# Performance work log

Measured on AMD Instinct MI355X. Metric: run time of the kernel, lower is better.

The kernel has to match this reference:

```python
import jax, jax.numpy as jnp
import numpy as np

N_SAMPLES = 256   # n_samples from __init__
N_THIN = 10       # N from __init__
N_WORDS = 4096


def setup_inputs() -> dict:
    key = jax.random.key(0)
    k1, k2, k3 = jax.random.split(key, 3)
    # scale potentials so per-step weight deltas stay in a sane exp() range
    bigram = jax.random.normal(k1, (N_WORDS, N_WORDS), dtype=jnp.float32)
    start = jax.random.normal(k2, (N_WORDS,), dtype=jnp.float32)
    end = jax.random.normal(k3, (N_WORDS,), dtype=jnp.float32)
    return {"n_words": N_WORDS, "bigram": bigram, "start": start, "end": end}


def _mh_chain(bigram, start, end, n_words, chain_size, rng):
    # chain[0] = identity permutation (random_start=False)
    perm0 = jnp.arange(n_words, dtype=jnp.int32)
    w0 = bigram[perm0[:-1], perm0[1:]].sum() + start[perm0[0]] + end[perm0[-1]]

    def step(carry, k):
        perm, w_last = carry
        k_pos, k_cat, k_u = jax.random.split(k, 3)
        # pick a token to move, remove it -> perm2 of length n_words-1
        pos = jax.random.randint(k_pos, (), 0, n_words)
        to_move = perm[pos]
        j = jnp.arange(n_words - 1)
        perm2 = perm[j + (j >= pos).astype(j.dtype)]
        # insertion logits over n_words slots (self._probs, unnormalized log p)
        logits = jnp.zeros((n_words,), dtype=bigram.dtype)
        logits = logits.at[0].add(start[to_move]).at[-1].add(end[to_move])
        logits = logits.at[1:].add(bigram[perm2, to_move])   # left-neighbor term
        logits = logits.at[:-1].add(bigram[to_move, perm2])  # right-neighbor term
        p = jax.nn.softmax(logits)
        new_pos = jax.random.categorical(k_cat, logits)
        # insert to_move at new_pos
        jj = jnp.arange(n_words)
        shifted = perm2[jnp.clip(jj - (jj > new_pos).astype(jj.dtype), 0, n_words - 2)]
        sample = jnp.where(jj == new_pos, to_move, shifted).astype(perm.dtype)
        # new chain weight
        new_w = bigram[sample[:-1], sample[1:]].sum() + start[sample[0]] + end[sample[-1]]
        # MH accept ratio; removing to_move from sample recovers perm2, so the
        # reverse insertion distribution equals p -> ratio p[new_pos]/p[pos]
        acc = jnp.minimum(1.0, jnp.exp(new_w - w_last) * p[new_pos] / p[pos])
        accept = acc > jax.random.uniform(k_u, ())
        perm_next = jnp.where(accept, sample, perm)
        w_next = jnp.where(accept, new_w, w_last)
        return (perm_next, w_next), perm_next

    keys = jax.random.split(rng, chain_size - 1)
    _, perms = jax.lax.scan(step, (perm0, w0), keys)
    chain = jnp.concatenate([perm0[None, :], perms], axis=0)  # [chain_size, n_words]
    sel = jnp.arange(0, chain_size, N_THIN) + (N_THIN - 1)    # thin: every N-th state
    return chain[sel]


def reference(n_words, bigram, start, end):
    chain_size = N_SAMPLES * N_THIN
    rng = jax.random.key(42)
    return _mh_chain(bigram, start, end, n_words, chain_size, rng)
```

## Files before the change

kernel.cpp:

```cpp
#include <hip/hip_runtime.h>
#include <stdint.h>


#define NW 4096
#define NSTEPS 2559
#define NTHREADS 1024
#define NWAVES 16

typedef unsigned long long u64;
typedef uint32_t u32;
typedef unsigned short u16;

__device__ __forceinline__ u32 rotl32(u32 v, u32 r) { return (v << r) | (v >> (32u - r)); }

__device__ __forceinline__ void tf2x32(u32 k0, u32 k1, u32 x0, u32 x1, u32* o0, u32* o1) {
  u32 ks2 = k0 ^ k1 ^ 0x1BD11BDAu;
  x0 += k0; x1 += k1;
#define TFR(r0, r1, r2, r3)                      \
  x0 += x1; x1 = rotl32(x1, r0); x1 ^= x0;       \
  x0 += x1; x1 = rotl32(x1, r1); x1 ^= x0;       \
  x0 += x1; x1 = rotl32(x1, r2); x1 ^= x0;       \
  x0 += x1; x1 = rotl32(x1, r3); x1 ^= x0;
  TFR(13, 15, 26, 6)  x0 += k1;  x1 += ks2 + 1u;
  TFR(17, 29, 16, 24) x0 += ks2; x1 += k0 + 2u;
  TFR(13, 15, 26, 6)  x0 += k0;  x1 += k1 + 3u;
  TFR(17, 29, 16, 24) x0 += k1;  x1 += ks2 + 4u;
  TFR(13, 15, 26, 6)  x0 += ks2; x1 += k0 + 5u;
#undef TFR
  *o0 = x0; *o1 = x1;
}

__device__ __forceinline__ float unif01(u32 bits) {
  return __uint_as_float((bits >> 9) | 0x3f800000u) - 1.0f;
}

__device__ __forceinline__ u32 fkey(float f) {
  u32 b = __float_as_uint(f);
  return b ^ ((b >> 31) ? 0xFFFFFFFFu : 0x80000000u);
}


template <int CTRL>
__device__ __forceinline__ u32 dpp32(u32 v) {
  return (u32)__builtin_amdgcn_update_dpp(0, (int)v, CTRL, 0xF, 0xF, true);
}

template <int CTRL>
__device__ __forceinline__ void dppmax64(u32& hi, u32& lo) {
  u32 h2 = dpp32<CTRL>(hi);
  u32 l2 = dpp32<CTRL>(lo);
  bool g = (h2 > hi) || (h2 == hi && l2 > lo);
  hi = g ? h2 : hi;
  lo = g ? l2 : lo;
}

__device__ __forceinline__ u64 wave_max_u64(u64 key) {
  u32 lo = (u32)key, hi = (u32)(key >> 32);
  dppmax64<0x111>(hi, lo); dppmax64<0x112>(hi, lo);
  dppmax64<0x114>(hi, lo); dppmax64<0x118>(hi, lo);
  dppmax64<0x142>(hi, lo); dppmax64<0x143>(hi, lo);
  return ((u64)hi << 32) | lo;
}

__device__ __forceinline__ u64 bfly16_max_u64(u64 key) {
  u32 lo = (u32)key, hi = (u32)(key >> 32);
  dppmax64<0xB1>(hi, lo); dppmax64<0x4E>(hi, lo);
  dppmax64<0x141>(hi, lo); dppmax64<0x140>(hi, lo);
  return ((u64)hi << 32) | lo;
}


#define TT 32
__global__ void transpose_k(const float* __restrict__ in, float* __restrict__ out) {
  __shared__ float tile[TT][TT + 1];
  int x = blockIdx.x * TT + threadIdx.x;
  int y = blockIdx.y * TT + threadIdx.y;
  for (int j = 0; j < TT; j += 8) tile[threadIdx.y + j][threadIdx.x] = in[(u64)(y + j) * NW + x];
  __syncthreads();
  x = blockIdx.y * TT + threadIdx.x;
  y = blockIdx.x * TT + threadIdx.y;
  for (int j = 0; j < TT; j += 8) out[(u64)(y + j) * NW + x] = tile[threadIdx.x][threadIdx.y + j];
}

__global__ void gumbel_k(float* __restrict__ gumb) {
  long long idx = (long long)blockIdx.x * blockDim.x + threadIdx.x;
  if (idx >= (long long)NSTEPS * NW) return;
  int t = (int)(idx >> 12);
  int i = (int)(idx & (NW - 1));
  u32 kt0, kt1, kc0, kc1, ba, bb;
  tf2x32(0u, 42u, 0u, (u32)t, &kt0, &kt1);
  tf2x32(kt0, kt1, 0u, 1u, &kc0, &kc1);
  tf2x32(kc0, kc1, 0u, (u32)i, &ba, &bb);
  float u = unif01(ba ^ bb);
  if (u == 0.0f) u = 1.17549435e-38f;
  float t1 = (float)log((double)u);
  float t2 = (float)log((double)(-t1));
  gumb[idx] = -t2;
}

__global__ void posu_k(int* __restrict__ posArr, float* __restrict__ uArr) {
  int t = blockIdx.x * blockDim.x + threadIdx.x;
  if (t >= NSTEPS) return;
  u32 kt0, kt1, kp0, kp1, ku0, ku1, k2a, k2b, ra, rb, ua, ub;
  tf2x32(0u, 42u, 0u, (u32)t, &kt0, &kt1);
  tf2x32(kt0, kt1, 0u, 0u, &kp0, &kp1);
  tf2x32(kt0, kt1, 0u, 2u, &ku0, &ku1);
  tf2x32(kp0, kp1, 0u, 1u, &k2a, &k2b);
  tf2x32(k2a, k2b, 0u, 0u, &ra, &rb);
  posArr[t] = (int)((ra ^ rb) & (u32)(NW - 1));
  tf2x32(ku0, ku1, 0u, 0u, &ua, &ub);
  uArr[t] = unif01(ua ^ ub);
}


#define SAMPLE_AT(idx)                                                        \
  ((idx) < np ? (int)s_perm[(idx) + ((idx) >= pos)]                           \
              : ((idx) == np ? tm                                             \
                             : (int)s_perm[((idx)-1) + (((idx)-1) >= pos)]))

__global__ __launch_bounds__(NTHREADS)
void mcmc_fast13(const float* __restrict__ bigram,
                 const float* __restrict__ bigT,
                 const float* __restrict__ gumb,
                 const int* __restrict__ posArr,
                 const float* __restrict__ uArr,
                 const float* __restrict__ startv,
                 const float* __restrict__ endv,
                 int* __restrict__ out) {
  __shared__ u16    s_perm[NW];
  __shared__ float2 s_rows[NW];
  __shared__ float  s_pairw[NW];
  __shared__ u64    s_redu[NWAVES];
  __shared__ float  s_stm, s_etm, s_lpos, s_brgS, s_vn1, s_vn2;
  __shared__ int    s_accs, s_tmA;

  const int tid = threadIdx.x;
  const int lane = tid & 63;
  const int wid = tid >> 6;
  const int j0 = tid * 4;

  for (int i = tid; i < NW; i += NTHREADS) s_perm[i] = (u16)i;
  ushort4 pq = make_ushort4((u16)j0, (u16)(j0 + 1), (u16)(j0 + 2), (u16)(j0 + 3));
  float4 pwq;
  pwq.x = bigram[(u64)j0 * NW + (j0 + 1)];
  pwq.y = bigram[(u64)(j0 + 1) * NW + (j0 + 2)];
  pwq.z = bigram[(u64)(j0 + 2) * NW + (j0 + 3)];
  pwq.w = (j0 + 3 < NW - 1) ? bigram[(u64)(j0 + 3) * NW + (j0 + 4)] : 0.0f;
  ((float4*)s_pairw)[tid] = pwq;

  int pos = posArr[0];
  int pn1 = posArr[1];
  float u_cur = uArr[0];
  float un1 = uArr[1];
  int tm = pos;
  {
    float4 rb4 = ((const float4*)(bigram + (u64)tm * NW))[tid];
    float4 rt4 = ((const float4*)(bigT + (u64)tm * NW))[tid];
    ((float4*)(&s_rows[j0]))[0] = make_float4(rt4.x, rb4.x, rt4.y, rb4.y);
    ((float4*)(&s_rows[j0]))[1] = make_float4(rt4.z, rb4.z, rt4.w, rb4.w);
  }
  if (tid == 0) { s_stm = startv[tm]; s_etm = endv[tm]; }

  float start_cur = startv[0];
  float end_cur = endv[NW - 1];

  float4 g4 = ((const float4*)gumb)[tid];
  __syncthreads();

  for (int t = 0; t < NSTEPS; ++t) {
    const float gg[4] = {g4.x, g4.y, g4.z, g4.w};
    const int tmR = (int)s_perm[pn1];
    const float4 rbR = ((const float4*)(bigram + (u64)tmR * NW))[tid];
    const float4 rtR = ((const float4*)(bigT + (u64)tmR * NW))[tid];
    float stmR = 0.0f, etmR = 0.0f;
    if (tid == 0) { stmR = startv[tmR]; etmR = endv[tmR]; }
    int pn2; float un2;
    {
      int tn = (t + 1 < NSTEPS) ? (t + 1) : (NSTEPS - 1);
      int tn2 = (t + 2 < NSTEPS) ? (t + 2) : (NSTEPS - 1);
      g4 = ((const float4*)(gumb + ((u64)tn << 12)))[tid];
      pn2 = posArr[tn2];
      un2 = uArr[tn2];
    }
    float stm_r = 0.0f, etm_r = 0.0f, remL = 0.0f, remR = 0.0f, brgv = 0.0f;
    float sv0m = 0.0f, ev1m = 0.0f;
    if (wid == 0) {
      stm_r = s_stm; etm_r = s_etm;
      int pl = (pos > 0) ? (int)s_perm[pos - 1] : 0;
      int pr = (pos < NW - 1) ? (int)s_perm[pos + 1] : 0;
      if (pos > 0)      remL = s_rows[pl].x;
      if (pos < NW - 1) remR = s_rows[pr].y;
      if (pos > 0 && pos < NW - 1) brgv = bigram[(u64)pl * NW + pr];
      sv0m = startv[(int)s_perm[(0 >= pos) ? 1 : 0]];
      ev1m = endv[(int)s_perm[(NW - 2) + ((NW - 2) >= pos)]];
      if (lane == 0) s_brgS = brgv;
    }

    const int p0i = pq.x, p1i = pq.y, p2i = pq.z, p3i = pq.w;
    int pm1, pp4;
    {
      u32 lo = (u32)pq.x | ((u32)pq.y << 16);
      u32 hi = (u32)pq.z | ((u32)pq.w << 16);
      pm1 = (int)(dpp32<0x138>(hi) >> 16);
      pp4 = (int)(dpp32<0x130>(lo) & 0xFFFFu);
      if (lane == 0)  pm1 = (tid > 0) ? (int)s_perm[j0 - 1] : 0;
      if (lane == 63) pp4 = (tid < NTHREADS - 1) ? (int)s_perm[j0 + 4] : 0;
    }
    float pwm1_e = 0.0f, pwp4_e = 0.0f;
    if (lane == 0 && tid > 0) pwm1_e = s_pairw[j0 - 1];
    if (lane == 63 && tid < NTHREADS - 1) pwp4_e = s_pairw[j0 + 4];

    const int w0 = (j0     >= pos) ? p1i : p0i;
    const int w1 = (j0 + 1 >= pos) ? p2i : p1i;
    const int w2 = (j0 + 2 >= pos) ? p3i : p2i;
    const int w3 = (j0 + 3 >= pos) ? pp4 : p3i;
    const int wprev = ((j0 - 1) >= pos) ? p0i : pm1;
    const float2 f0 = s_rows[w0];
    const float2 f1 = s_rows[w1];
    const float2 f2 = s_rows[w2];
    const float2 f3 = s_rows[w3];
    float tprev = __uint_as_float(dpp32<0x138>(__float_as_uint(f3.x)));
    if (lane == 0 && tid > 0) tprev = s_rows[wprev].x;
    float li0 = tprev + f0.y;
    float li1 = f0.x + f1.y;
    float li2 = f1.x + f2.y;
    float li3 = f2.x + f3.y;
    if (tid == 0)            li0 = s_stm + f0.y;
    if (tid == NTHREADS - 1) li3 = s_etm + f2.x;
    if ((pos >> 2) == tid) {
      int k = pos & 3;
      s_lpos = (k == 0) ? li0 : ((k == 1) ? li1 : ((k == 2) ? li2 : li3));
    }
    u64 best;
    {
      u64 b0 = ((u64)fkey(gg[0] + li0) << 32) | (u32)(NW - 1 - j0);
      u64 b1 = ((u64)fkey(gg[1] + li1) << 32) | (u32)(NW - 2 - j0);
      u64 b2 = ((u64)fkey(gg[2] + li2) << 32) | (u32)(NW - 3 - j0);
      u64 b3 = ((u64)fkey(gg[3] + li3) << 32) | (u32)(NW - 4 - j0);
      best = b0 > b1 ? b0 : b1;
      u64 b23 = b2 > b3 ? b2 : b3;
      if (b23 > best) best = b23;
    }
    best = wave_max_u64(best);
    if (lane == 63) s_redu[wid] = best;
    __syncthreads();

    if (wid == 0) {
      u64 bb = bfly16_max_u64(s_redu[lane & 15]);
      const int np = NW - 1 - (int)(bb & 0xFFFFFFFFu);
      int ls_i = (np >= 1) ? ((np - 1) + ((np - 1) >= pos)) : 0;
      int rs_i = (np <= NW - 2) ? (np + (np >= pos)) : 0;
      const int l_s = (int)s_perm[ls_i];
      const int r_s = (int)s_perm[rs_i];
      const int tmA = SAMPLE_AT(pn1);
      float splitv = 0.0f;
      if (np > 0 && np < NW - 1) {
        int k_s = (np - 1) + ((np - 1) >= pos);
        splitv = (np == pos) ? brgv : s_pairw[k_s];
      }
      float vnpm1 = (np >= 1)      ? s_rows[l_s].x : 0.0f;
      float vnp   = (np <= NW - 2) ? s_rows[r_s].y : 0.0f;
      float sv0 = (np > 0) ? sv0m : stm_r;
      float ev1 = (np < NW - 1) ? ev1m : etm_r;
      float lposv = s_lpos;
      double delta = 0.0;
      if (pos > 0)                 delta -= (double)remL;
      if (pos < NW - 1)            delta -= (double)remR;
      if (pos > 0 && pos < NW - 1) delta += (double)brgv;
      if (np > 0)                  delta += (double)vnpm1;
      if (np < NW - 1)             delta += (double)vnp;
      if (np > 0 && np < NW - 1)   delta -= (double)splitv;
      delta += ((double)sv0 - (double)start_cur) + ((double)ev1 - (double)end_cur);
      float lnp = (np == 0) ? (stm_r + vnp)
                : ((np == NW - 1) ? (etm_r + vnpm1) : (vnpm1 + vnp));
      double ed = delta + ((double)lnp - (double)lposv);
      float a = fminf(1.0f, expf((float)ed));
      int acc = (a > u_cur) ? 1 : 0;
      if (lane == 0) { s_accs = acc; s_vn1 = vnpm1; s_vn2 = vnp; s_tmA = tmA; }
      if (acc) { start_cur = sv0; end_cur = ev1; }
    }
    __syncthreads();

    const int acc = s_accs;
    int tm_next = tmR;
    float4 rb = rbR, rt = rtR;
    ushort4 st = pq;
    if (acc) {
      tm_next = s_tmA;
      rb = ((const float4*)(bigram + (u64)tm_next * NW))[tid];
      rt = ((const float4*)(bigT + (u64)tm_next * NW))[tid];
      u64 bb = bfly16_max_u64(s_redu[lane & 15]);
      const int np = NW - 1 - (int)(bb & 0xFFFFFFFFu);
      st.x = (j0     < np) ? (u16)w0 : ((j0     == np) ? (u16)tm : (u16)wprev);
      st.y = (j0 + 1 < np) ? (u16)w1 : ((j0 + 1 == np) ? (u16)tm : (u16)w0);
      st.z = (j0 + 2 < np) ? (u16)w2 : ((j0 + 2 == np) ? (u16)tm : (u16)w1);
      st.w = (j0 + 3 < np) ? (u16)w3 : ((j0 + 3 == np) ? (u16)tm : (u16)w2);
      ((ushort4*)s_perm)[tid] = st;
      float pwm1 = __uint_as_float(dpp32<0x138>(__float_as_uint(pwq.w)));
      float pwp4 = __uint_as_float(dpp32<0x130>(__float_as_uint(pwq.x)));
      if (lane == 0)  pwm1 = pwm1_e;
      if (lane == 63) pwp4 = pwp4_e;
      const float brgAll = s_brgS;
      float nv0, nv1, nv2, nv3;
      {
        float vA0 = (j0     < pos - 1) ? pwq.x : pwq.y;
        float vB0 = (j0 - 1 < pos - 1) ? pwm1  : pwq.x;
        nv0 = (j0 < np) ? vA0 : vB0;
        int kk0 = (j0 < np) ? j0 : j0 - 1;
        if (kk0 == pos - 1) nv0 = brgAll;

        float vA1 = (j0 + 1 < pos - 1) ? pwq.y : pwq.z;
        float vB1 = (j0     < pos - 1) ? pwq.x : pwq.y;
        nv1 = (j0 + 1 < np) ? vA1 : vB1;
        int kk1 = (j0 + 1 < np) ? j0 + 1 : j0;
        if (kk1 == pos - 1) nv1 = brgAll;

        float vA2 = (j0 + 2 < pos - 1) ? pwq.z : pwq.w;
        float vB2 = (j0 + 1 < pos - 1) ? pwq.y : pwq.z;
        nv2 = (j0 + 2 < np) ? vA2 : vB2;
        int kk2 = (j0 + 2 < np) ? j0 + 2 : j0 + 1;
        if (kk2 == pos - 1) nv2 = brgAll;

        float vA3 = (j0 + 3 < pos - 1) ? pwq.w : pwp4;
        float vB3 = (j0 + 2 < pos - 1) ? pwq.z : pwq.w;
        nv3 = (j0 + 3 < np) ? vA3 : vB3;
        int kk3 = (j0 + 3 < np) ? j0 + 3 : j0 + 2;
        if (kk3 == pos - 1) nv3 = brgAll;
      }
      const float vn1 = s_vn1, vn2 = s_vn2;
      float o0 = (j0     == np - 1) ? vn1 : ((j0     == np) ? vn2 : nv0);
      float o1 = (j0 + 1 == np - 1) ? vn1 : ((j0 + 1 == np) ? vn2 : nv1);
      float o2 = (j0 + 2 == np - 1) ? vn1 : ((j0 + 2 == np) ? vn2 : nv2);
      float o3 = (j0 + 3 == np - 1) ? vn1 : ((j0 + 3 == np) ? vn2 : nv3);
      if (j0 + 3 >= NW - 1) o3 = 0.0f;
      pwq = make_float4(o0, o1, o2, o3);
      ((float4*)s_pairw)[tid] = pwq;
      if (tid == 0) { s_stm = startv[tm_next]; s_etm = endv[tm_next]; }
    } else {
      if (tid == 0) { s_stm = stmR; s_etm = etmR; }
    }
    ((float4*)(&s_rows[j0]))[0] = make_float4(rt.x, rb.x, rt.y, rb.y);
    ((float4*)(&s_rows[j0]))[1] = make_float4(rt.z, rb.z, rt.w, rb.w);
    pq = st;
    tm = tm_next;
    pos = pn1; u_cur = un1;
    pn1 = pn2; un1 = un2;

    if ((t % 10) == 8) {
      int row = (t - 8) / 10;
      int4 o4;
      o4.x = (int)pq.x; o4.y = (int)pq.y; o4.z = (int)pq.z; o4.w = (int)pq.w;
      ((int4*)(out + (u64)row * NW))[tid] = o4;
    }
    __syncthreads();
  }
}


__global__ __launch_bounds__(NTHREADS)
void mcmc_kernel(const float* __restrict__ bigram,
                 const float* __restrict__ startv,
                 const float* __restrict__ endv,
                 int* __restrict__ out) {
  __shared__ int    s_perm[NW];
  __shared__ float  s_logit[NW];
  __shared__ float  s_gath[NW];
  __shared__ float  s_redf[NWAVES];
  __shared__ u64    s_redu[NWAVES];
  __shared__ double s_redd[NWAVES];
  __shared__ float  s_m, s_Z, s_w;
  __shared__ int    s_pos, s_tm, s_np, s_acc;
  __shared__ u32    s_kcat0, s_kcat1, s_ku0, s_ku1;

  const int tid = threadIdx.x;
  const int lane = tid & 63;
  const int wid = tid >> 6;

  for (int i = tid; i < NW; i += NTHREADS) s_perm[i] = i;
  for (int j = tid; j < NW - 1; j += NTHREADS) s_gath[j] = bigram[(u64)j * NW + (j + 1)];
  __syncthreads();
  if (tid == 0) {
    float S = 0.0f;
    for (int j = 0; j < NW - 1; ++j) S += s_gath[j];
    S = S + startv[0];
    S = S + endv[NW - 1];
    s_w = S;
  }
  __syncthreads();

  for (int t = 0; t < NSTEPS; ++t) {
    if (tid == 0) {
      u32 kt0, kt1;
      tf2x32(0u, 42u, 0u, (u32)t, &kt0, &kt1);
      u32 kp0, kp1, kc0, kc1, ku0, ku1;
      tf2x32(kt0, kt1, 0u, 0u, &kp0, &kp1);
      tf2x32(kt0, kt1, 0u, 1u, &kc0, &kc1);
      tf2x32(kt0, kt1, 0u, 2u, &ku0, &ku1);
      u32 k2a, k2b, ra, rb;
      tf2x32(kp0, kp1, 0u, 1u, &k2a, &k2b);
      tf2x32(k2a, k2b, 0u, 0u, &ra, &rb);
      int pos = (int)((ra ^ rb) & (u32)(NW - 1));
      s_pos = pos;
      s_tm = s_perm[pos];
      s_kcat0 = kc0; s_kcat1 = kc1; s_ku0 = ku0; s_ku1 = ku1;
    }
    __syncthreads();
    const int pos = s_pos, tm = s_tm;

    float lmax = -3.402823466e+38f;
    for (int i = tid; i < NW; i += NTHREADS) {
      float li;
      if (i == 0) {
        int r = s_perm[(0 >= pos) ? 1 : 0];
        li = startv[tm] + bigram[(u64)tm * NW + r];
      } else if (i == NW - 1) {
        int l = s_perm[((NW - 2) >= pos) ? (NW - 1) : (NW - 2)];
        li = endv[tm] + bigram[(u64)l * NW + tm];
      } else {
        int l = s_perm[((i - 1) >= pos) ? i : (i - 1)];
        int r = s_perm[(i >= pos) ? (i + 1) : i];
        li = bigram[(u64)l * NW + tm] + bigram[(u64)tm * NW + r];
      }
      s_logit[i] = li;
      lmax = fmaxf(lmax, li);
    }
    for (int o = 32; o > 0; o >>= 1) lmax = fmaxf(lmax, __shfl_down(lmax, o, 64));
    if (lane == 0) s_redf[wid] = lmax;
    __syncthreads();
    if (tid == 0) {
      float m = s_redf[0];
      for (int w = 1; w < NWAVES; ++w) m = fmaxf(m, s_redf[w]);
      s_m = m;
    }
    __syncthreads();
    const float m = s_m;

    double zacc = 0.0;
    u64 best = 0;
    const u32 kc0 = s_kcat0, kc1 = s_kcat1;
    for (int i = tid; i < NW; i += NTHREADS) {
      float li = s_logit[i];
      float ex = (float)exp((double)(li - m));
      zacc += (double)ex;
      u32 ba, bb;
      tf2x32(kc0, kc1, 0u, (u32)i, &ba, &bb);
      float u = unif01(ba ^ bb);
      if (u == 0.0f) u = 1.17549435e-38f;
      float t1 = (float)log((double)u);
      float t2 = (float)log((double)(-t1));
      float g = -t2;
      float sv = g + li;
      u64 key = ((u64)fkey(sv) << 32) | (u32)(NW - 1 - i);
      if (key > best) best = key;
    }
    for (int o = 32; o > 0; o >>= 1) {
      u64 w = __shfl_down(best, o, 64);
      if (w > best) best = w;
      zacc += __shfl_down(zacc, o, 64);
    }
    if (lane == 0) { s_redu[wid] = best; s_redd[wid] = zacc; }
    __syncthreads();
    if (tid == 0) {
      u64 b = s_redu[0]; double z = s_redd[0];
      for (int w = 1; w < NWAVES; ++w) {
        if (s_redu[w] > b) b = s_redu[w];
        z += s_redd[w];
      }
      s_np = NW - 1 - (int)(b & 0xFFFFFFFFu);
      s_Z = (float)z;
    }
    __syncthreads();
    const int np = s_np;

    for (int j = tid; j < NW - 1; j += NTHREADS) {
      int a = (j < np) ? s_perm[j + (j >= pos)]
                       : ((j == np) ? tm : s_perm[(j - 1) + ((j - 1) >= pos)]);
      int j1 = j + 1;
      int b = (j1 < np) ? s_perm[j1 + (j1 >= pos)]
                        : ((j1 == np) ? tm : s_perm[(j1 - 1) + ((j1 - 1) >= pos)]);
      s_gath[j] = bigram[(u64)a * NW + b];
    }
    __syncthreads();

    if (tid == 0) {
      float S = 0.0f;
      for (int j = 0; j < NW - 1; ++j) S += s_gath[j];
      int s0 = (0 < np) ? s_perm[(0 >= pos) ? 1 : 0] : tm;
      int sl = ((NW - 1) == np) ? tm : s_perm[(NW - 2) + ((NW - 2) >= pos)];
      S = S + startv[s0];
      S = S + endv[sl];
      float dw = S - s_w;
      float e1 = (float)exp((double)dw);
      float en = (float)exp((double)(s_logit[np] - m));
      float eo = (float)exp((double)(s_logit[pos] - m));
      float pn = en / s_Z;
      float po = eo / s_Z;
      float acc = e1 * pn;
      acc = acc / po;
      acc = fminf(1.0f, acc);
      u32 ua, ub;
      tf2x32(s_ku0, s_ku1, 0u, 0u, &ua, &ub);
      float u = unif01(ua ^ ub);
      int accept = (acc > u) ? 1 : 0;
      s_acc = accept;
      if (accept) s_w = S;
    }
    __syncthreads();

    int stash[4];
    if (s_acc) {
      for (int k = 0; k < 4; ++k) {
        int i = tid + k * NTHREADS;
        stash[k] = (i < np) ? s_perm[i + (i >= pos)]
                            : ((i == np) ? tm : s_perm[(i - 1) + ((i - 1) >= pos)]);
      }
    }
    __syncthreads();
    if (s_acc) {
      for (int k = 0; k < 4; ++k) {
        int i = tid + k * NTHREADS;
        s_perm[i] = stash[k];
      }
    }
    __syncthreads();

    if (((t + 1) % 10) == 9) {
      int row = (t - 8) / 10;
      for (int i = tid; i < NW; i += NTHREADS) out[(u64)row * NW + i] = s_perm[i];
    }
    __syncthreads();
  }
}

extern "C" void kernel_launch(void* const* d_in, const int* in_sizes, int n_in,
                              void* d_out, int out_size, void* d_ws, size_t ws_size,
                              hipStream_t stream) {
  const float* bigram = (const float*)d_in[1];
  const float* startv = (const float*)d_in[2];
  const float* endv   = (const float*)d_in[3];
  int* out = (int*)d_out;

  const size_t needT = (size_t)NW * NW * sizeof(float);
  const size_t needG = (size_t)NSTEPS * NW * sizeof(float);
  const size_t needP = (size_t)NSTEPS * (sizeof(int) + sizeof(float));

  if (ws_size >= needT + needG + needP) {
    float* bigT = (float*)d_ws;
    float* gumb = (float*)((char*)d_ws + needT);
    int* posArr = (int*)((char*)d_ws + needT + needG);
    float* uArr = (float*)((char*)d_ws + needT + needG + (size_t)NSTEPS * sizeof(int));
    hipLaunchKernelGGL(transpose_k, dim3(NW / TT, NW / TT), dim3(TT, 8), 0, stream,
                       bigram, bigT);
    long long ng = (long long)NSTEPS * NW;
    hipLaunchKernelGGL(gumbel_k, dim3((unsigned)((ng + 255) / 256)), dim3(256), 0, stream,
                       gumb);
    hipLaunchKernelGGL(posu_k, dim3((NSTEPS + 255) / 256), dim3(256), 0, stream,
                       posArr, uArr);
    hipLaunchKernelGGL(mcmc_fast13, dim3(1), dim3(NTHREADS), 0, stream,
                       bigram, bigT, gumb, posArr, uArr, startv, endv, out);
  } else {
    hipLaunchKernelGGL(mcmc_kernel, dim3(1), dim3(NTHREADS), 0, stream,
                       bigram, startv, endv, out);
  }
}
```

Before: 6.604 ms.

## Double-buffer shared state and compute accept decision redundantly to drop a barrier

Shared permutation, row and pair-weight arrays are double-buffered so each step reads the current buffer and writes the next one. Every thread now repeats the final reduction and the accept/reject computation instead of wave 0 doing it and broadcasting. This removes one __syncthreads per step and the shared scalars used to pass state between waves. The per-thread argmax is also simplified to a float compare before building a single 64-bit key. In exchange, every wave issues the extra global loads (bigram bridge, start/end) and the double-precision delta math, and shared memory use roughly doubles.

```diff
diff --git a/kernel.cpp b/kernel.cpp
--- a/kernel.cpp
+++ b/kernel.cpp
@@ -113,13 +113,8 @@
 }
 
 
-#define SAMPLE_AT(idx)                                                        \
-  ((idx) < np ? (int)s_perm[(idx) + ((idx) >= pos)]                           \
-              : ((idx) == np ? tm                                             \
-                             : (int)s_perm[((idx)-1) + (((idx)-1) >= pos)]))
-
 __global__ __launch_bounds__(NTHREADS)
-void mcmc_fast13(const float* __restrict__ bigram,
+void mcmc_fast14(const float* __restrict__ bigram,
                  const float* __restrict__ bigT,
                  const float* __restrict__ gumb,
                  const int* __restrict__ posArr,
@@ -127,26 +122,27 @@
                  const float* __restrict__ startv,
                  const float* __restrict__ endv,
                  int* __restrict__ out) {
-  __shared__ u16    s_perm[NW];
-  __shared__ float2 s_rows[NW];
-  __shared__ float  s_pairw[NW];
+  __shared__ u16    s_permB[2][NW];
+  __shared__ float2 s_rowsB[2][NW];
+  __shared__ float  s_pairwB[2][NW];
   __shared__ u64    s_redu[NWAVES];
-  __shared__ float  s_stm, s_etm, s_lpos, s_brgS, s_vn1, s_vn2;
-  __shared__ int    s_accs, s_tmA;
+  __shared__ float  s_lpos;
 
   const int tid = threadIdx.x;
   const int lane = tid & 63;
   const int wid = tid >> 6;
   const int j0 = tid * 4;
 
-  for (int i = tid; i < NW; i += NTHREADS) s_perm[i] = (u16)i;
+  int pc = 0, rc = 0, qc = 0;
+
+  for (int i = tid; i < NW; i += NTHREADS) s_permB[0][i] = (u16)i;
   ushort4 pq = make_ushort4((u16)j0, (u16)(j0 + 1), (u16)(j0 + 2), (u16)(j0 + 3));
   float4 pwq;
   pwq.x = bigram[(u64)j0 * NW + (j0 + 1)];
   pwq.y = bigram[(u64)(j0 + 1) * NW + (j0 + 2)];
   pwq.z = bigram[(u64)(j0 + 2) * NW + (j0 + 3)];
   pwq.w = (j0 + 3 < NW - 1) ? bigram[(u64)(j0 + 3) * NW + (j0 + 4)] : 0.0f;
-  ((float4*)s_pairw)[tid] = pwq;
+  ((float4*)s_pairwB[0])[tid] = pwq;
 
   int pos = posArr[0];
   int pn1 = posArr[1];
@@ -156,11 +152,11 @@
   {
     float4 rb4 = ((const float4*)(bigram + (u64)tm * NW))[tid];
     float4 rt4 = ((const float4*)(bigT + (u64)tm * NW))[tid];
-    ((float4*)(&s_rows[j0]))[0] = make_float4(rt4.x, rb4.x, rt4.y, rb4.y);
-    ((float4*)(&s_rows[j0]))[1] = make_float4(rt4.z, rb4.z, rt4.w, rb4.w);
+    ((float4*)(&s_rowsB[0][j0]))[0] = make_float4(rt4.x, rb4.x, rt4.y, rb4.y);
+    ((float4*)(&s_rowsB[0][j0]))[1] = make_float4(rt4.z, rb4.z, rt4.w, rb4.w);
   }
-  if (tid == 0) { s_stm = startv[tm]; s_etm = endv[tm]; }
-
+  float stm_cur = startv[tm];
+  float etm_cur = endv[tm];
   float start_cur = startv[0];
   float end_cur = endv[NW - 1];
 
@@ -168,12 +164,11 @@
   __syncthreads();
 
   for (int t = 0; t < NSTEPS; ++t) {
+    const u16*    permC  = s_permB[pc];
+    const float2* rowsC  = s_rowsB[rc];
+    const float*  pairwC = s_pairwB[qc];
+
     const float gg[4] = {g4.x, g4.y, g4.z, g4.w};
-    const int tmR = (int)s_perm[pn1];
-    const float4 rbR = ((const float4*)(bigram + (u64)tmR * NW))[tid];
-    const float4 rtR = ((const float4*)(bigT + (u64)tmR * NW))[tid];
-    float stmR = 0.0f, etmR = 0.0f;
-    if (tid == 0) { stmR = startv[tmR]; etmR = endv[tmR]; }
     int pn2; float un2;
     {
       int tn = (t + 1 < NSTEPS) ? (t + 1) : (NSTEPS - 1);
@@ -182,19 +177,18 @@
       pn2 = posArr[tn2];
       un2 = uArr[tn2];
     }
-    float stm_r = 0.0f, etm_r = 0.0f, remL = 0.0f, remR = 0.0f, brgv = 0.0f;
-    float sv0m = 0.0f, ev1m = 0.0f;
-    if (wid == 0) {
-      stm_r = s_stm; etm_r = s_etm;
-      int pl = (pos > 0) ? (int)s_perm[pos - 1] : 0;
-      int pr = (pos < NW - 1) ? (int)s_perm[pos + 1] : 0;
-      if (pos > 0)      remL = s_rows[pl].x;
-      if (pos < NW - 1) remR = s_rows[pr].y;
-      if (pos > 0 && pos < NW - 1) brgv = bigram[(u64)pl * NW + pr];
-      sv0m = startv[(int)s_perm[(0 >= pos) ? 1 : 0]];
-      ev1m = endv[(int)s_perm[(NW - 2) + ((NW - 2) >= pos)]];
-      if (lane == 0) s_brgS = brgv;
-    }
+    const int tmR = (int)permC[pn1];
+    const float4 rbR = ((const float4*)(bigram + (u64)tmR * NW))[tid];
+    const float4 rtR = ((const float4*)(bigT + (u64)tmR * NW))[tid];
+    const float stmR = startv[tmR];
+    const float etmR = endv[tmR];
+    const int pl = (pos > 0) ? (int)permC[pos - 1] : 0;
+    const int pr = (pos < NW - 1) ? (int)permC[pos + 1] : 0;
+    const float remL = (pos > 0) ? rowsC[pl].x : 0.0f;
+    const float remR = (pos < NW - 1) ? rowsC[pr].y : 0.0f;
+    const float brgv = (pos > 0 && pos < NW - 1) ? bigram[(u64)pl * NW + pr] : 0.0f;
+    const float sv0m = startv[(int)permC[(0 >= pos) ? 1 : 0]];
+    const float ev1m = endv[(int)permC[(NW - 2) + ((NW - 2) >= pos)]];
 
     const int p0i = pq.x, p1i = pq.y, p2i = pq.z, p3i = pq.w;
     int pm1, pp4;
@@ -203,145 +197,146 @@
       u32 hi = (u32)pq.z | ((u32)pq.w << 16);
       pm1 = (int)(dpp32<0x138>(hi) >> 16);
       pp4 = (int)(dpp32<0x130>(lo) & 0xFFFFu);
-      if (lane == 0)  pm1 = (tid > 0) ? (int)s_perm[j0 - 1] : 0;
-      if (lane == 63) pp4 = (tid < NTHREADS - 1) ? (int)s_perm[j0 + 4] : 0;
+      if (lane == 0)  pm1 = (tid > 0) ? (int)permC[j0 - 1] : 0;
+      if (lane == 63) pp4 = (tid < NTHREADS - 1) ? (int)permC[j0 + 4] : 0;
     }
     float pwm1_e = 0.0f, pwp4_e = 0.0f;
-    if (lane == 0 && tid > 0) pwm1_e = s_pairw[j0 - 1];
-    if (lane == 63 && tid < NTHREADS - 1) pwp4_e = s_pairw[j0 + 4];
+    if (lane == 0 && tid > 0) pwm1_e = pairwC[j0 - 1];
+    if (lane == 63 && tid < NTHREADS - 1) pwp4_e = pairwC[j0 + 4];
 
     const int w0 = (j0     >= pos) ? p1i : p0i;
     const int w1 = (j0 + 1 >= pos) ? p2i : p1i;
     const int w2 = (j0 + 2 >= pos) ? p3i : p2i;
     const int w3 = (j0 + 3 >= pos) ? pp4 : p3i;
     const int wprev = ((j0 - 1) >= pos) ? p0i : pm1;
-    const float2 f0 = s_rows[w0];
-    const float2 f1 = s_rows[w1];
-    const float2 f2 = s_rows[w2];
-    const float2 f3 = s_rows[w3];
+    const float2 f0 = rowsC[w0];
+    const float2 f1 = rowsC[w1];
+    const float2 f2 = rowsC[w2];
+    const float2 f3 = rowsC[w3];
     float tprev = __uint_as_float(dpp32<0x138>(__float_as_uint(f3.x)));
-    if (lane == 0 && tid > 0) tprev = s_rows[wprev].x;
+    if (lane == 0 && tid > 0) tprev = rowsC[wprev].x;
     float li0 = tprev + f0.y;
     float li1 = f0.x + f1.y;
     float li2 = f1.x + f2.y;
     float li3 = f2.x + f3.y;
-    if (tid == 0)            li0 = s_stm + f0.y;
-    if (tid == NTHREADS - 1) li3 = s_etm + f2.x;
+    if (tid == 0)            li0 = stm_cur + f0.y;
+    if (tid == NTHREADS - 1) li3 = etm_cur + f2.x;
     if ((pos >> 2) == tid) {
       int k = pos & 3;
       s_lpos = (k == 0) ? li0 : ((k == 1) ? li1 : ((k == 2) ? li2 : li3));
     }
-    u64 best;
     {
-      u64 b0 = ((u64)fkey(gg[0] + li0) << 32) | (u32)(NW - 1 - j0);
-      u64 b1 = ((u64)fkey(gg[1] + li1) << 32) | (u32)(NW - 2 - j0);
-      u64 b2 = ((u64)fkey(gg[2] + li2) << 32) | (u32)(NW - 3 - j0);
-      u64 b3 = ((u64)fkey(gg[3] + li3) << 32) | (u32)(NW - 4 - j0);
-      best = b0 > b1 ? b0 : b1;
-      u64 b23 = b2 > b3 ? b2 : b3;
-      if (b23 > best) best = b23;
-    }
-    best = wave_max_u64(best);
-    if (lane == 63) s_redu[wid] = best;
-    __syncthreads();
-
-    if (wid == 0) {
-      u64 bb = bfly16_max_u64(s_redu[lane & 15]);
-      const int np = NW - 1 - (int)(bb & 0xFFFFFFFFu);
-      int ls_i = (np >= 1) ? ((np - 1) + ((np - 1) >= pos)) : 0;
-      int rs_i = (np <= NW - 2) ? (np + (np >= pos)) : 0;
-      const int l_s = (int)s_perm[ls_i];
-      const int r_s = (int)s_perm[rs_i];
-      const int tmA = SAMPLE_AT(pn1);
-      float splitv = 0.0f;
-      if (np > 0 && np < NW - 1) {
-        int k_s = (np - 1) + ((np - 1) >= pos);
-        splitv = (np == pos) ? brgv : s_pairw[k_s];
-      }
-      float vnpm1 = (np >= 1)      ? s_rows[l_s].x : 0.0f;
-      float vnp   = (np <= NW - 2) ? s_rows[r_s].y : 0.0f;
-      float sv0 = (np > 0) ? sv0m : stm_r;
-      float ev1 = (np < NW - 1) ? ev1m : etm_r;
-      float lposv = s_lpos;
-      double delta = 0.0;
-      if (pos > 0)                 delta -= (double)remL;
-      if (pos < NW - 1)            delta -= (double)remR;
-      if (pos > 0 && pos < NW - 1) delta += (double)brgv;
-      if (np > 0)                  delta += (double)vnpm1;
-      if (np < NW - 1)             delta += (double)vnp;
-      if (np > 0 && np < NW - 1)   delta -= (double)splitv;
-      delta += ((double)sv0 - (double)start_cur) + ((double)ev1 - (double)end_cur);
-      float lnp = (np == 0) ? (stm_r + vnp)
-                : ((np == NW - 1) ? (etm_r + vnpm1) : (vnpm1 + vnp));
-      double ed = delta + ((double)lnp - (double)lposv);
-      float a = fminf(1.0f, expf((float)ed));
-      int acc = (a > u_cur) ? 1 : 0;
-      if (lane == 0) { s_accs = acc; s_vn1 = vnpm1; s_vn2 = vnp; s_tmA = tmA; }
-      if (acc) { start_cur = sv0; end_cur = ev1; }
-    }
-    __syncthreads();
-
-    const int acc = s_accs;
-    int tm_next = tmR;
-    float4 rb = rbR, rt = rtR;
+      float sv0_ = gg[0] + li0;
+      float sv1_ = gg[1] + li1;
+      float sv2_ = gg[2] + li2;
+      float sv3_ = gg[3] + li3;
+      float mx = sv0_; int ix = j0;
+      if (sv1_ > mx) { mx = sv1_; ix = j0 + 1; }
+      if (sv2_ > mx) { mx = sv2_; ix = j0 + 2; }
+      if (sv3_ > mx) { mx = sv3_; ix = j0 + 3; }
+      u64 key = ((u64)fkey(mx) << 32) | (u32)(NW - 1 - ix);
+      key = wave_max_u64(key);
+      if (lane == 63) s_redu[wid] = key;
+    }
+    __syncthreads();
+
+    u64 bb = bfly16_max_u64(s_redu[lane & 15]);
+    const int np = NW - 1 - (int)(bb & 0xFFFFFFFFu);
+    const int ls_i = (np >= 1) ? ((np - 1) + ((np - 1) >= pos)) : 0;
+    const int rs_i = (np <= NW - 2) ? (np + (np >= pos)) : 0;
+    const int l_s = (int)permC[ls_i];
+    const int r_s = (int)permC[rs_i];
+    const int tmA = (pn1 < np) ? (int)permC[pn1 + (pn1 >= pos)]
+                  : ((pn1 == np) ? tm : (int)permC[(pn1 - 1) + ((pn1 - 1) >= pos)]);
+    float splitv = 0.0f;
+    if (np > 0 && np < NW - 1) {
+      int k_s = (np - 1) + ((np - 1) >= pos);
+      splitv = (np == pos) ? brgv : pairwC[k_s];
+    }
+    const float vnpm1 = (np >= 1)      ? rowsC[l_s].x : 0.0f;
+    const float vnp   = (np <= NW - 2) ? rowsC[r_s].y : 0.0f;
+    const float sv0 = (np > 0) ? sv0m : stm_cur;
+    const float ev1 = (np < NW - 1) ? ev1m : etm_cur;
+    const float lposv = s_lpos;
+    double delta = 0.0;
+    if (pos > 0)                 delta -= (double)remL;
+    if (pos < NW - 1)            delta -= (double)remR;
+    if (pos > 0 && pos < NW - 1) delta += (double)brgv;
+    if (np > 0)                  delta += (double)vnpm1;
+    if (np < NW - 1)             delta += (double)vnp;
+    if (np > 0 && np < NW - 1)   delta -= (double)splitv;
+    delta += ((double)sv0 - (double)start_cur) + ((double)ev1 - (double)end_cur);
+    const float lnp = (np == 0) ? (stm_cur + vnp)
+                    : ((np == NW - 1) ? (etm_cur + vnpm1) : (vnpm1 + vnp));
+    const double ed = delta + ((double)lnp - (double)lposv);
+    const float a = fminf(1.0f, expf((float)ed));
+    const int acc = (a > u_cur) ? 1 : 0;
+    if (acc) { start_cur = sv0; end_cur = ev1; }
+
+    int tm_next;
+    float4 rb, rt;
+    float stmN, etmN;
     ushort4 st = pq;
+    float4 npw = pwq;
     if (acc) {
-      tm_next = s_tmA;
+      tm_next = tmA;
       rb = ((const float4*)(bigram + (u64)tm_next * NW))[tid];
       rt = ((const float4*)(bigT + (u64)tm_next * NW))[tid];
-      u64 bb = bfly16_max_u64(s_redu[lane & 15]);
-      const int np = NW - 1 - (int)(bb & 0xFFFFFFFFu);
+      stmN = startv[tm_next];
+      etmN = endv[tm_next];
       st.x = (j0     < np) ? (u16)w0 : ((j0     == np) ? (u16)tm : (u16)wprev);
       st.y = (j0 + 1 < np) ? (u16)w1 : ((j0 + 1 == np) ? (u16)tm : (u16)w0);
       st.z = (j0 + 2 < np) ? (u16)w2 : ((j0 + 2 == np) ? (u16)tm : (u16)w1);
       st.w = (j0 + 3 < np) ? (u16)w3 : ((j0 + 3 == np) ? (u16)tm : (u16)w2);
-      ((ushort4*)s_perm)[tid] = st;
+      ((ushort4*)s_permB[pc ^ 1])[tid] = st;
       float pwm1 = __uint_as_float(dpp32<0x138>(__float_as_uint(pwq.w)));
       float pwp4 = __uint_as_float(dpp32<0x130>(__float_as_uint(pwq.x)));
       if (lane == 0)  pwm1 = pwm1_e;
       if (lane == 63) pwp4 = pwp4_e;
-      const float brgAll = s_brgS;
       float nv0, nv1, nv2, nv3;
       {
         float vA0 = (j0     < pos - 1) ? pwq.x : pwq.y;
         float vB0 = (j0 - 1 < pos - 1) ? pwm1  : pwq.x;
         nv0 = (j0 < np) ? vA0 : vB0;
         int kk0 = (j0 < np) ? j0 : j0 - 1;
-        if (kk0 == pos - 1) nv0 = brgAll;
+        if (kk0 == pos - 1) nv0 = brgv;
 
         float vA1 = (j0 + 1 < pos - 1) ? pwq.y : pwq.z;
         float vB1 = (j0     < pos - 1) ? pwq.x : pwq.y;
         nv1 = (j0 + 1 < np) ? vA1 : vB1;
         int kk1 = (j0 + 1 < np) ? j0 + 1 : j0;
-        if (kk1 == pos - 1) nv1 = brgAll;
+        if (kk1 == pos - 1) nv1 = brgv;
 
         float vA2 = (j0 + 2 < pos - 1) ? pwq.z : pwq.w;
         float vB2 = (j0 + 1 < pos - 1) ? pwq.y : pwq.z;
         nv2 = (j0 + 2 < np) ? vA2 : vB2;
         int kk2 = (j0 + 2 < np) ? j0 + 2 : j0 + 1;
-        if (kk2 == pos - 1) nv2 = brgAll;
+        if (kk2 == pos - 1) nv2 = brgv;
 
         float vA3 = (j0 + 3 < pos - 1) ? pwq.w : pwp4;
         float vB3 = (j0 + 2 < pos - 1) ? pwq.z : pwq.w;
         nv3 = (j0 + 3 < np) ? vA3 : vB3;
         int kk3 = (j0 + 3 < np) ? j0 + 3 : j0 + 2;
-        if (kk3 == pos - 1) nv3 = brgAll;
+        if (kk3 == pos - 1) nv3 = brgv;
       }
-      const float vn1 = s_vn1, vn2 = s_vn2;
-      float o0 = (j0     == np - 1) ? vn1 : ((j0     == np) ? vn2 : nv0);
-      float o1 = (j0 + 1 == np - 1) ? vn1 : ((j0 + 1 == np) ? vn2 : nv1);
-      float o2 = (j0 + 2 == np - 1) ? vn1 : ((j0 + 2 == np) ? vn2 : nv2);
-      float o3 = (j0 + 3 == np - 1) ? vn1 : ((j0 + 3 == np) ? vn2 : nv3);
+      float o0 = (j0     == np - 1) ? vnpm1 : ((j0     == np) ? vnp : nv0);
+      float o1 = (j0 + 1 == np - 1) ? vnpm1 : ((j0 + 1 == np) ? vnp : nv1);
+      float o2 = (j0 + 2 == np - 1) ? vnpm1 : ((j0 + 2 == np) ? vnp : nv2);
+      float o3 = (j0 + 3 == np - 1) ? vnpm1 : ((j0 + 3 == np) ? vnp : nv3);
       if (j0 + 3 >= NW - 1) o3 = 0.0f;
-      pwq = make_float4(o0, o1, o2, o3);
-      ((float4*)s_pairw)[tid] = pwq;
-      if (tid == 0) { s_stm = startv[tm_next]; s_etm = endv[tm_next]; }
+      npw = make_float4(o0, o1, o2, o3);
+      ((float4*)s_pairwB[qc ^ 1])[tid] = npw;
+      pc ^= 1; qc ^= 1;
     } else {
-      if (tid == 0) { s_stm = stmR; s_etm = etmR; }
-    }
-    ((float4*)(&s_rows[j0]))[0] = make_float4(rt.x, rb.x, rt.y, rb.y);
-    ((float4*)(&s_rows[j0]))[1] = make_float4(rt.z, rb.z, rt.w, rb.w);
-    pq = st;
+      tm_next = tmR;
+      rb = rbR; rt = rtR;
+      stmN = stmR; etmN = etmR;
+    }
+    ((float4*)(&s_rowsB[rc ^ 1][j0]))[0] = make_float4(rt.x, rb.x, rt.y, rb.y);
+    ((float4*)(&s_rowsB[rc ^ 1][j0]))[1] = make_float4(rt.z, rb.z, rt.w, rb.w);
+    rc ^= 1;
+    pq = st; pwq = npw;
+    stm_cur = stmN; etm_cur = etmN;
     tm = tm_next;
     pos = pn1; u_cur = un1;
     pn1 = pn2; un1 = un2;
@@ -556,7 +551,7 @@
                        gumb);
     hipLaunchKernelGGL(posu_k, dim3((NSTEPS + 255) / 256), dim3(256), 0, stream,
                        posArr, uArr);
-    hipLaunchKernelGGL(mcmc_fast13, dim3(1), dim3(NTHREADS), 0, stream,
+    hipLaunchKernelGGL(mcmc_fast14, dim3(1), dim3(NTHREADS), 0, stream,
                        bigram, bigT, gumb, posArr, uArr, startv, endv, out);
   } else {
     hipLaunchKernelGGL(mcmc_kernel, dim3(1), dim3(NTHREADS), 0, stream,
```

Measured after the change: 7.335 ms. +11.1%, slower.

## Use lightweight LDS-only barriers, split row cache, 32-bit wave argmax

Applied to the files above, without the earlier changes.

Replaces __syncthreads with a barrier that waits only on LDS counters (lgkmcnt), so outstanding global prefetch loads (next row, gumbel noise) are not drained at each of the three per-step barriers. The interleaved float2 row cache is split into two separate float arrays. The per-wave argmax is changed from a 64-bit DPP max to a 32-bit max followed by a ballot to recover the winning index. The lighter barrier relies on global loads not being needed across it; the ballot-based tie handling picks the lowest lane, which must match the original tie-break order.

```diff
diff --git a/kernel.cpp b/kernel.cpp
--- a/kernel.cpp
+++ b/kernel.cpp
@@ -39,10 +39,23 @@
   return b ^ ((b >> 31) ? 0xFFFFFFFFu : 0x80000000u);
 }
 
+__device__ __forceinline__ void light_bar() {
+  asm volatile("s_waitcnt lgkmcnt(0)" ::: "memory");
+  __builtin_amdgcn_s_barrier();
+  __builtin_amdgcn_sched_barrier(0);
+  asm volatile("" ::: "memory");
+}
+
 
 template <int CTRL>
 __device__ __forceinline__ u32 dpp32(u32 v) {
   return (u32)__builtin_amdgcn_update_dpp(0, (int)v, CTRL, 0xF, 0xF, true);
+}
+
+template <int CTRL>
+__device__ __forceinline__ u32 dppumax(u32 v) {
+  u32 s = dpp32<CTRL>(v);
+  return (v > s) ? v : s;
 }
 
 template <int CTRL>
@@ -52,14 +65,6 @@
   bool g = (h2 > hi) || (h2 == hi && l2 > lo);
   hi = g ? h2 : hi;
   lo = g ? l2 : lo;
-}
-
-__device__ __forceinline__ u64 wave_max_u64(u64 key) {
-  u32 lo = (u32)key, hi = (u32)(key >> 32);
-  dppmax64<0x111>(hi, lo); dppmax64<0x112>(hi, lo);
-  dppmax64<0x114>(hi, lo); dppmax64<0x118>(hi, lo);
-  dppmax64<0x142>(hi, lo); dppmax64<0x143>(hi, lo);
-  return ((u64)hi << 32) | lo;
 }
 
 __device__ __forceinline__ u64 bfly16_max_u64(u64 key) {
@@ -119,7 +124,7 @@
                              : (int)s_perm[((idx)-1) + (((idx)-1) >= pos)]))
 
 __global__ __launch_bounds__(NTHREADS)
-void mcmc_fast13(const float* __restrict__ bigram,
+void mcmc_fast16(const float* __restrict__ bigram,
                  const float* __restrict__ bigT,
                  const float* __restrict__ gumb,
                  const int* __restrict__ posArr,
@@ -128,7 +133,8 @@
                  const float* __restrict__ endv,
                  int* __restrict__ out) {
   __shared__ u16    s_perm[NW];
-  __shared__ float2 s_rows[NW];
+  __shared__ float  s_rowT[NW];
+  __shared__ float  s_rowB[NW];
   __shared__ float  s_pairw[NW];
   __shared__ u64    s_redu[NWAVES];
   __shared__ float  s_stm, s_etm, s_lpos, s_brgS, s_vn1, s_vn2;
@@ -156,8 +162,8 @@
   {
     float4 rb4 = ((const float4*)(bigram + (u64)tm * NW))[tid];
     float4 rt4 = ((const float4*)(bigT + (u64)tm * NW))[tid];
-    ((float4*)(&s_rows[j0]))[0] = make_float4(rt4.x, rb4.x, rt4.y, rb4.y);
-    ((float4*)(&s_rows[j0]))[1] = make_float4(rt4.z, rb4.z, rt4.w, rb4.w);
+    ((float4*)s_rowB)[tid] = rb4;
+    ((float4*)s_rowT)[tid] = rt4;
   }
   if (tid == 0) { s_stm = startv[tm]; s_etm = endv[tm]; }
 
@@ -188,8 +194,8 @@
       stm_r = s_stm; etm_r = s_etm;
       int pl = (pos > 0) ? (int)s_perm[pos - 1] : 0;
       int pr = (pos < NW - 1) ? (int)s_perm[pos + 1] : 0;
-      if (pos > 0)      remL = s_rows[pl].x;
-      if (pos < NW - 1) remR = s_rows[pr].y;
+      if (pos > 0)      remL = s_rowT[pl];
+      if (pos < NW - 1) remR = s_rowB[pr];
       if (pos > 0 && pos < NW - 1) brgv = bigram[(u64)pl * NW + pr];
       sv0m = startv[(int)s_perm[(0 >= pos) ? 1 : 0]];
       ev1m = endv[(int)s_perm[(NW - 2) + ((NW - 2) >= pos)]];
@@ -215,35 +221,46 @@
     const int w2 = (j0 + 2 >= pos) ? p3i : p2i;
     const int w3 = (j0 + 3 >= pos) ? pp4 : p3i;
     const int wprev = ((j0 - 1) >= pos) ? p0i : pm1;
-    const float2 f0 = s_rows[w0];
-    const float2 f1 = s_rows[w1];
-    const float2 f2 = s_rows[w2];
-    const float2 f3 = s_rows[w3];
-    float tprev = __uint_as_float(dpp32<0x138>(__float_as_uint(f3.x)));
-    if (lane == 0 && tid > 0) tprev = s_rows[wprev].x;
-    float li0 = tprev + f0.y;
-    float li1 = f0.x + f1.y;
-    float li2 = f1.x + f2.y;
-    float li3 = f2.x + f3.y;
-    if (tid == 0)            li0 = s_stm + f0.y;
-    if (tid == NTHREADS - 1) li3 = s_etm + f2.x;
+    const float t0v = s_rowT[w0];
+    const float t1v = s_rowT[w1];
+    const float t2v = s_rowT[w2];
+    const float t3v = s_rowT[w3];
+    const float b0v = s_rowB[w0];
+    const float b1v = s_rowB[w1];
+    const float b2v = s_rowB[w2];
+    const float b3v = s_rowB[w3];
+    float tprev = __uint_as_float(dpp32<0x138>(__float_as_uint(t3v)));
+    if (lane == 0 && tid > 0) tprev = s_rowT[wprev];
+    float li0 = tprev + b0v;
+    float li1 = t0v + b1v;
+    float li2 = t1v + b2v;
+    float li3 = t2v + b3v;
+    if (tid == 0)            li0 = s_stm + b0v;
+    if (tid == NTHREADS - 1) li3 = s_etm + t2v;
     if ((pos >> 2) == tid) {
       int k = pos & 3;
       s_lpos = (k == 0) ? li0 : ((k == 1) ? li1 : ((k == 2) ? li2 : li3));
     }
-    u64 best;
     {
-      u64 b0 = ((u64)fkey(gg[0] + li0) << 32) | (u32)(NW - 1 - j0);
-      u64 b1 = ((u64)fkey(gg[1] + li1) << 32) | (u32)(NW - 2 - j0);
-      u64 b2 = ((u64)fkey(gg[2] + li2) << 32) | (u32)(NW - 3 - j0);
-      u64 b3 = ((u64)fkey(gg[3] + li3) << 32) | (u32)(NW - 4 - j0);
-      best = b0 > b1 ? b0 : b1;
-      u64 b23 = b2 > b3 ? b2 : b3;
-      if (b23 > best) best = b23;
-    }
-    best = wave_max_u64(best);
-    if (lane == 63) s_redu[wid] = best;
-    __syncthreads();
+      float sv0_ = gg[0] + li0;
+      float sv1_ = gg[1] + li1;
+      float sv2_ = gg[2] + li2;
+      float sv3_ = gg[3] + li3;
+      float mx = sv0_; int ix = j0;
+      if (sv1_ > mx) { mx = sv1_; ix = j0 + 1; }
+      if (sv2_ > mx) { mx = sv2_; ix = j0 + 2; }
+      if (sv3_ > mx) { mx = sv3_; ix = j0 + 3; }
+      u32 kloc = fkey(mx);
+      u32 kr = kloc;
+      kr = dppumax<0x111>(kr); kr = dppumax<0x112>(kr);
+      kr = dppumax<0x114>(kr); kr = dppumax<0x118>(kr);
+      kr = dppumax<0x142>(kr); kr = dppumax<0x143>(kr);
+      u32 kmax = (u32)__builtin_amdgcn_readlane((int)kr, 63);
+      u64 mask = __ballot(kloc == kmax);
+      int wl = (int)(__ffsll((long long)mask)) - 1;
+      if (lane == wl) s_redu[wid] = ((u64)kmax << 32) | (u32)(NW - 1 - ix);
+    }
+    light_bar();
 
     if (wid == 0) {
       u64 bb = bfly16_max_u64(s_redu[lane & 15]);
@@ -258,8 +275,8 @@
         int k_s = (np - 1) + ((np - 1) >= pos);
         splitv = (np == pos) ? brgv : s_pairw[k_s];
       }
-      float vnpm1 = (np >= 1)      ? s_rows[l_s].x : 0.0f;
-      float vnp   = (np <= NW - 2) ? s_rows[r_s].y : 0.0f;
+      float vnpm1 = (np >= 1)      ? s_rowT[l_s] : 0.0f;
+      float vnp   = (np <= NW - 2) ? s_rowB[r_s] : 0.0f;
       float sv0 = (np > 0) ? sv0m : stm_r;
       float ev1 = (np < NW - 1) ? ev1m : etm_r;
       float lposv = s_lpos;
@@ -279,7 +296,7 @@
       if (lane == 0) { s_accs = acc; s_vn1 = vnpm1; s_vn2 = vnp; s_tmA = tmA; }
       if (acc) { start_cur = sv0; end_cur = ev1; }
     }
-    __syncthreads();
+    light_bar();
 
     const int acc = s_accs;
     int tm_next = tmR;
@@ -339,8 +356,8 @@
     } else {
       if (tid == 0) { s_stm = stmR; s_etm = etmR; }
     }
-    ((float4*)(&s_rows[j0]))[0] = make_float4(rt.x, rb.x, rt.y, rb.y);
-    ((float4*)(&s_rows[j0]))[1] = make_float4(rt.z, rb.z, rt.w, rb.w);
+    ((float4*)s_rowB)[tid] = rb;
+    ((float4*)s_rowT)[tid] = rt;
     pq = st;
     tm = tm_next;
     pos = pn1; u_cur = un1;
@@ -352,7 +369,7 @@
       o4.x = (int)pq.x; o4.y = (int)pq.y; o4.z = (int)pq.z; o4.w = (int)pq.w;
       ((int4*)(out + (u64)row * NW))[tid] = o4;
     }
-    __syncthreads();
+    light_bar();
   }
 }
 
@@ -556,7 +573,7 @@
                        gumb);
     hipLaunchKernelGGL(posu_k, dim3((NSTEPS + 255) / 256), dim3(256), 0, stream,
                        posArr, uArr);
-    hipLaunchKernelGGL(mcmc_fast13, dim3(1), dim3(NTHREADS), 0, stream,
+    hipLaunchKernelGGL(mcmc_fast16, dim3(1), dim3(NTHREADS), 0, stream,
                        bigram, bigT, gumb, posArr, uArr, startv, endv, out);
   } else {
     hipLaunchKernelGGL(mcmc_kernel, dim3(1), dim3(NTHREADS), 0, stream,
```

New measurement: 6.496 ms. No clear change (-1.6%).
